# Kernel optimization log

Hardware: AMD Instinct MI355X
Metric: run time of the kernel (lower is better)

## Reference

```python
import jax, jax.numpy as jnp
import numpy as np

B, P, T, R, A = 16384, 3, 2, 3, 3   # batch, n_players, teammates, rivals, action_dim
HID = [1024, 512]
ENC_OUT = 64
RIVAL_START = 9 * 9 + 12 * P       # 117, as in the torch module
NEG_SLOPE = 0.01                    # nn.LeakyReLU default


def _linpack(key, k, din, dout):
    # PyTorch nn.Linear default init: U(-1/sqrt(din), 1/sqrt(din))
    kw, kb = jax.random.split(key)
    bound = 1.0 / np.sqrt(din)
    W = jax.random.uniform(kw, (k, din, dout), jnp.float32, -bound, bound)
    b = jax.random.uniform(kb, (k, dout), jnp.float32, -bound, bound)
    return W, b


def setup_inputs() -> dict:
    key = jax.random.key(0)
    ks = jax.random.split(key, 16)
    obs = jax.random.normal(ks[0], (B, P, 144), jnp.float32)
    act = jax.random.normal(ks[1], (B, P, A), jnp.float32)
    # stacked per-segment encoder weights (grouped small GEMMs)
    Wp1, bp1 = _linpack(ks[2], 9, 2 + A, 32)
    Wp2, bp2 = _linpack(ks[3], 9, 32, ENC_OUT)
    Wt1, bt1 = _linpack(ks[4], T, 12, 32)
    Wt2, bt2 = _linpack(ks[5], T, 32, ENC_OUT)
    Wr1, br1 = _linpack(ks[6], R, 9, 32)
    Wr2, br2 = _linpack(ks[7], R, 32, ENC_OUT)
    # q head: [P*896] -> 1024 -> 512 -> P
    din = P * (9 + T + R) * ENC_OUT
    Wq1, bq1 = _linpack(ks[8], 1, din, HID[0]);  Wq1, bq1 = Wq1[0], bq1[0]
    Wq2, bq2 = _linpack(ks[9], 1, HID[0], HID[1]); Wq2, bq2 = Wq2[0], bq2[0]
    Wq3, bq3 = _linpack(ks[10], 1, HID[1], P);   Wq3, bq3 = Wq3[0], bq3[0]
    return dict(obs=obs, act=act,
                Wp1=Wp1, bp1=bp1, Wp2=Wp2, bp2=bp2,
                Wt1=Wt1, bt1=bt1, Wt2=Wt2, bt2=bt2,
                Wr1=Wr1, br1=br1, Wr2=Wr2, br2=br2,
                Wq1=Wq1, bq1=bq1, Wq2=Wq2, bq2=bq2, Wq3=Wq3, bq3=bq3)


def _enc2(x, W1, b1, W2, b2):
    # x: [B, P, K, din]; W1: [K, din, 32]; W2: [K, 32, 64] -> [B, P, K, 64]
    lrelu = lambda v: jax.nn.leaky_relu(v, NEG_SLOPE)
    h = lrelu(jnp.einsum('bpki,kio->bpko', x, W1) + b1)
    return lrelu(jnp.einsum('bpkh,kho->bpko', h, W2) + b2)


def reference(obs, act, Wp1, bp1, Wp2, bp2, Wt1, bt1, Wt2, bt2,
              Wr1, br1, Wr2, br2, Wq1, bq1, Wq2, bq2, Wq3, bq3):
    b = obs.shape[0]
    # prop segments: obs[:, :, 2i:2i+2] concat act  -> [B, P, 9, 2+A]
    x_prop = jnp.concatenate(
        [obs[:, :, :18].reshape(b, P, 9, 2),
         jnp.broadcast_to(act[:, :, None, :], (b, P, 9, A))], axis=-1)
    x_team = obs[:, :, 18:18 + 12 * T].reshape(b, P, T, 12)
    x_riv = obs[:, :, RIVAL_START:RIVAL_START + 9 * R].reshape(b, P, R, 9)
    ep = _enc2(x_prop, Wp1, bp1, Wp2, bp2)   # [B, P, 9, 64]
    et = _enc2(x_team, Wt1, bt1, Wt2, bt2)   # [B, P, T, 64]
    er = _enc2(x_riv, Wr1, br1, Wr2, br2)    # [B, P, R, 64]
    enc = jnp.concatenate([ep, et, er], axis=2).reshape(b, -1)  # [B, P*14*64]
    # q head: ReLU hidden activations, identity output
    h = jax.nn.relu(enc @ Wq1 + bq1)
    h = jax.nn.relu(h @ Wq2 + bq2)
    return h @ Wq3 + bq3                      # [B, P]
```

## Files before the change

kernel.cpp:

```cpp
#include <hip/hip_runtime.h>
#include <hip/hip_bf16.h>
#include <cstdint>

typedef __bf16 bf16x8 __attribute__((ext_vector_type(8)));
typedef float f32x4 __attribute__((ext_vector_type(4)));

__device__ __forceinline__ void gld16(const __bf16* g, __bf16* lds) {
    __builtin_amdgcn_global_load_lds(
        (__attribute__((address_space(1))) void*)(uintptr_t)g,
        (__attribute__((address_space(3))) void*)(uint32_t)(uintptr_t)lds,
        16, 0, 0);
}

__global__ __launch_bounds__(256) void transpose_bf16_k(const float* __restrict__ in,
                                                        __bf16* __restrict__ out,
                                                        int R, int C) {
    __shared__ float t[64][65];
    const int r0 = blockIdx.x * 64, c0 = blockIdx.y * 64;
    const int tid = threadIdx.x;
#pragma unroll
    for (int i = 0; i < 16; i++) {
        int idx = i * 256 + tid;
        int rr = idx >> 6, cc = idx & 63;
        t[rr][cc] = in[(size_t)(r0 + rr) * C + (c0 + cc)];
    }
    __syncthreads();
#pragma unroll
    for (int i = 0; i < 16; i++) {
        int idx = i * 256 + tid;
        int rr = idx >> 6, cc = idx & 63;
        out[(size_t)(c0 + rr) * R + (r0 + cc)] = (__bf16)t[cc][rr];
    }
}

__global__ __launch_bounds__(256) void pack_weights(const float* __restrict__ Wp1, const float* __restrict__ bp1,
                                                    const float* __restrict__ Wp2, const float* __restrict__ bp2,
                                                    const float* __restrict__ Wt1, const float* __restrict__ bt1,
                                                    const float* __restrict__ Wt2, const float* __restrict__ bt2,
                                                    const float* __restrict__ Wr1, const float* __restrict__ br1,
                                                    const float* __restrict__ Wr2, const float* __restrict__ br2,
                                                    float* __restrict__ w1p, __bf16* __restrict__ w2t) {
    const int s = blockIdx.x, tid = threadIdx.x;
    int ks, din, w1off;
    const float *W1, *B1, *W2, *B2;
    if (s < 9)      { ks = s;      din = 5;  w1off = s * 160;
                      W1 = Wp1; B1 = bp1; W2 = Wp2; B2 = bp2; }
    else if (s < 11){ ks = s - 9;  din = 12; w1off = 1440 + ks * 384;
                      W1 = Wt1; B1 = bt1; W2 = Wt2; B2 = bt2; }
    else            { ks = s - 11; din = 9;  w1off = 2208 + ks * 288;
                      W1 = Wr1; B1 = br1; W2 = Wr2; B2 = br2; }
    W1 += ks * din * 32; B1 += ks * 32; W2 += ks * 2048; B2 += ks * 64;
    for (int i = tid; i < din * 32; i += 256) w1p[w1off + i] = W1[i];
    if (tid < 32) w1p[3072 + s * 32 + tid] = B1[tid];
    if (tid < 64) w1p[3520 + s * 64 + tid] = B2[tid];
    for (int i = tid; i < 2048; i += 256) {
        const int o = i >> 5, k = i & 31;
        w2t[s * 2048 + i] = (__bf16)W2[k * 64 + o];
    }
}

__global__ __launch_bounds__(256) void enc_fused(const float* __restrict__ obs,
                                                 const float* __restrict__ act,
                                                 const float* __restrict__ w1p,
                                                 const __bf16* __restrict__ w2t,
                                                 __bf16* __restrict__ enc) {
    __shared__ float sW[4416];
    __shared__ __bf16 sH[2][64 * 40];
    const int tid = threadIdx.x;
    for (int i = tid; i < 4416; i += 256) sW[i] = w1p[i];
    const int rloc = tid >> 2, q = tid & 3;
    const int row = blockIdx.x * 64 + rloc;
    const float* orow = obs + (size_t)row * 144;
    const float a0 = act[row * 3], a1 = act[row * 3 + 1], a2 = act[row * 3 + 2];
    const int wv = tid >> 6, lane = tid & 63;
    const int fr = lane & 15, kq = lane >> 4;
    __syncthreads();
    int buf = 0;

    auto l2 = [&](int s) {
        __syncthreads();
        bf16x8 bfr[4];
#pragma unroll
        for (int n = 0; n < 4; n++)
            bfr[n] = *(const bf16x8*)&w2t[(s * 64 + n * 16 + fr) * 32 + kq * 8];
        const bf16x8 afr = *(const bf16x8*)&sH[buf][(wv * 16 + fr) * 40 + kq * 8];
        f32x4 acc[4] = {};
#pragma unroll
        for (int n = 0; n < 4; n++)
            acc[n] = __builtin_amdgcn_mfma_f32_16x16x32_bf16(afr, bfr[n], acc[n], 0, 0, 0);
        const float* b2 = sW + 3520 + s * 64;
        const size_t rG = (size_t)blockIdx.x * 64 + wv * 16 + kq * 4;
#pragma unroll
        for (int n = 0; n < 4; n++) {
            const float bv = b2[n * 16 + fr];
#pragma unroll
            for (int rg = 0; rg < 4; rg++) {
                float v = acc[n][rg] + bv;
                v = fmaxf(v, 0.01f * v);
                enc[(rG + rg) * 896 + s * 64 + n * 16 + fr] = (__bf16)v;
            }
        }
        buf ^= 1;
    };

#define L1(DIN, W1OFF, SGI, XLOAD)                                   \
    {                                                                \
        float x[DIN];                                                \
        XLOAD;                                                       \
        const float* w1 = sW + (W1OFF);                              \
        const float* b1 = sW + 3072 + (SGI) * 32;                    \
        bf16x8 t_;                                                   \
        _Pragma("unroll") for (int j = 0; j < 8; j++) {              \
            const int o = q * 8 + j;                                 \
            float a_ = b1[o];                                        \
            _Pragma("unroll") for (int i = 0; i < DIN; i++)          \
                a_ += x[i] * w1[i * 32 + o];                         \
            t_[j] = (__bf16)fmaxf(a_, 0.01f * a_);                   \
        }                                                            \
        *(bf16x8*)&sH[buf][rloc * 40 + q * 8] = t_;                  \
    }

    for (int k = 0; k < 9; k++) {
        L1(5, k * 160, k,
           { x[0] = orow[2 * k]; x[1] = orow[2 * k + 1]; x[2] = a0; x[3] = a1; x[4] = a2; })
        l2(k);
    }
    for (int k = 0; k < 2; k++) {
        L1(12, 1440 + k * 384, 9 + k,
           { _Pragma("unroll") for (int i = 0; i < 12; i++) x[i] = orow[18 + 12 * k + i]; })
        l2(9 + k);
    }
    for (int k = 0; k < 3; k++) {
        L1(9, 2208 + k * 288, 11 + k,
           { _Pragma("unroll") for (int i = 0; i < 9; i++) x[i] = orow[117 + 9 * k + i]; })
        l2(11 + k);
    }
#undef L1
}

template <int NB>
__global__ __launch_bounds__(512, 2) void gemm256_relu(const __bf16* __restrict__ Ag,
                                                       const __bf16* __restrict__ Btg,
                                                       const float* __restrict__ bias,
                                                       __bf16* __restrict__ Cg,
                                                       int N, int K, int lgn) {
    __shared__ __align__(16) __bf16 ldsA[2][2][128 * 64];
    __shared__ __align__(16) __bf16 ldsB[2][2][NB * 64 * 64];
    const int tid = threadIdx.x;
    const int wid = tid >> 6, lane = tid & 63;
    const int wm = wid >> 2, wn = wid & 3;
    const int fr = lane & 15, kq = lane >> 4;

    const int chunk = gridDim.x >> 3;
    const int wg = (blockIdx.x & 7) * chunk + (blockIdx.x >> 3);
    const int bn = wg & ((1 << lgn) - 1), bm = wg >> lgn;

    const int c0 = tid, c1 = tid + 512;
    const int r0 = c0 >> 3, s0 = (c0 & 7) ^ (r0 & 7);
    const int r1 = c1 >> 3, s1 = (c1 & 7) ^ (r1 & 7);
    const size_t aH = (size_t)128 * K;
    const size_t bH = (size_t)(NB * 64) * K;
    const __bf16* aB0 = Ag + (size_t)(bm * 256 + r0) * K + s0 * 8;
    const __bf16* aB1 = Ag + (size_t)(bm * 256 + r1) * K + s1 * 8;
    const __bf16* bB0 = Btg + (size_t)(bn * (NB * 128) + r0) * K + s0 * 8;
    const __bf16* bB1 = Btg + (size_t)(bn * (NB * 128) + r1) * K + s1 * 8;

    f32x4 acc[2][2][4][NB] = {};
    bf16x8 a0[4][2], a1[4][2], b0[NB][2], b1[NB][2];

#define STAGE_A(BUF, H, KO)                                   \
    do {                                                      \
        __bf16* d_ = &ldsA[BUF][H][0];                        \
        gld16(aB0 + (H)*aH + (KO), d_ + c0 * 8);              \
        gld16(aB1 + (H)*aH + (KO), d_ + c1 * 8);              \
    } while (0)
#define STAGE_B(BUF, H, KO)                                   \
    do {                                                      \
        __bf16* d_ = &ldsB[BUF][H][0];                        \
        gld16(bB0 + (H)*bH + (KO), d_ + c0 * 8);              \
        if constexpr (NB == 2) gld16(bB1 + (H)*bH + (KO), d_ + c1 * 8); \
    } while (0)

#define LDFA(BUF, H, ROW, KS) \
    (*(const bf16x8*)&ldsA[BUF][H][(ROW) * 64 + ((((KS)*4 + kq) ^ ((ROW)&7)) * 8)])
#define LDFB(BUF, H, ROW, KS) \
    (*(const bf16x8*)&ldsB[BUF][H][(ROW) * 64 + ((((KS)*4 + kq) ^ ((ROW)&7)) * 8)])

#define LOAD_A(BUF, H, DST)                                   \
    _Pragma("unroll") for (int m = 0; m < 4; m++)             \
        _Pragma("unroll") for (int ks = 0; ks < 2; ks++)      \
            DST[m][ks] = LDFA(BUF, H, wm * 64 + m * 16 + fr, ks);
#define LOAD_B(BUF, H, DST)                                   \
    _Pragma("unroll") for (int n = 0; n < NB; n++)            \
        _Pragma("unroll") for (int ks = 0; ks < 2; ks++)      \
            DST[n][ks] = LDFB(BUF, H, wn * (NB * 16) + n * 16 + fr, ks);

#define MM(Q, R, AR, BR)                                      \
    __builtin_amdgcn_s_setprio(1);                            \
    _Pragma("unroll") for (int ks = 0; ks < 2; ks++)          \
        _Pragma("unroll") for (int m = 0; m < 4; m++)         \
            _Pragma("unroll") for (int n = 0; n < NB; n++)    \
                acc[Q][R][m][n] = __builtin_amdgcn_mfma_f32_16x16x32_bf16( \
                    AR[m][ks], BR[n][ks], acc[Q][R][m][n], 0, 0, 0); \
    __builtin_amdgcn_s_setprio(0);

#define SB0 __builtin_amdgcn_sched_barrier(0)
#define BAR __builtin_amdgcn_s_barrier()
#define LGKM_B1                                               \
    if constexpr (NB == 2) asm volatile("s_waitcnt lgkmcnt(4)" ::: "memory"); \
    else asm volatile("s_waitcnt lgkmcnt(2)" ::: "memory");
#define LGKM(NSTR) asm volatile("s_waitcnt lgkmcnt(" NSTR ")" ::: "memory")
#define VMW(NSTR) asm volatile("s_waitcnt vmcnt(" NSTR ")" ::: "memory")
#define VMW2(N2, N1)                                          \
    if constexpr (NB == 2) VMW(#N2); else VMW(#N1);

    const int NT = K >> 6;

    STAGE_A(0, 0, 0);
    STAGE_B(0, 0, 0);
    STAGE_B(0, 1, 0);
    STAGE_A(0, 1, 0);
    VMW("2");
    BAR;
    LOAD_A(0, 0, a0)
    LOAD_B(0, 0, b0)
    SB0;

    for (int t = 0; t < NT - 1; ++t) {
        const int buf = t & 1, nb = buf ^ 1;
        const int kO = (t + 1) << 6;

        STAGE_A(nb, 0, kO);
        STAGE_B(nb, 0, kO);
        VMW2(4, 3);
        LOAD_B(buf, 1, b1)
        SB0;
        BAR;
        LGKM_B1;
        SB0;
        MM(0, 0, a0, b0)

        STAGE_B(nb, 1, kO);
        STAGE_A(nb, 1, kO);
        LOAD_A(buf, 1, a1)
        SB0;
        BAR;
        LGKM("8");
        SB0;
        MM(0, 1, a0, b1)

        BAR;
        LGKM("0");
        SB0;
        MM(1, 0, a1, b0)

        VMW("2");
        BAR;
        LOAD_A(nb, 0, a0)
        LOAD_B(nb, 0, b0)
        SB0;
        MM(1, 1, a1, b1)
    }

    {
        const int buf = (NT - 1) & 1;
        VMW("0");
        LOAD_B(buf, 1, b1)
        SB0;
        BAR;
        LGKM_B1;
        SB0;
        MM(0, 0, a0, b0)

        LOAD_A(buf, 1, a1)
        SB0;
        BAR;
        LGKM("8");
        SB0;
        MM(0, 1, a0, b1)

        BAR;
        LGKM("0");
        SB0;
        MM(1, 0, a1, b0)

        MM(1, 1, a1, b1)
    }

    const int cc = lane & 15, rr = (lane >> 4) << 2;
#pragma unroll
    for (int q = 0; q < 2; q++)
#pragma unroll
        for (int r2 = 0; r2 < 2; r2++)
#pragma unroll
            for (int m = 0; m < 4; m++)
#pragma unroll
                for (int n = 0; n < NB; n++) {
                    const int colG = bn * (NB * 128) + r2 * (NB * 64) + wn * (NB * 16) + n * 16 + cc;
                    const int rowG = bm * 256 + q * 128 + wm * 64 + m * 16 + rr;
                    const float bv = bias[colG];
#pragma unroll
                    for (int reg = 0; reg < 4; reg++) {
                        float v = acc[q][r2][m][n][reg] + bv;
                        v = fmaxf(v, 0.0f);
                        Cg[(size_t)(rowG + reg) * N + colG] = (__bf16)v;
                    }
                }
#undef STAGE_A
#undef STAGE_B
#undef LDFA
#undef LDFB
#undef LOAD_A
#undef LOAD_B
#undef MM
#undef SB0
#undef BAR
#undef LGKM_B1
#undef LGKM
#undef VMW
#undef VMW2
}

__global__ __launch_bounds__(256) void head_kernel(const __bf16* __restrict__ h2,
                                                   const float* __restrict__ Wq3,
                                                   const float* __restrict__ bq3,
                                                   float* __restrict__ out) {
    const int wave = threadIdx.x >> 6, lane = threadIdx.x & 63;
    const int row = blockIdx.x * 4 + wave;
    const bf16x8 hv = *(const bf16x8*)(h2 + (size_t)row * 512 + lane * 8);
    float s0 = 0.f, s1 = 0.f, s2 = 0.f;
#pragma unroll
    for (int i = 0; i < 8; i++) {
        const float hf = (float)hv[i];
        const int k = lane * 8 + i;
        s0 += hf * Wq3[k * 3 + 0];
        s1 += hf * Wq3[k * 3 + 1];
        s2 += hf * Wq3[k * 3 + 2];
    }
#pragma unroll
    for (int off = 32; off > 0; off >>= 1) {
        s0 += __shfl_xor(s0, off);
        s1 += __shfl_xor(s1, off);
        s2 += __shfl_xor(s2, off);
    }
    if (lane == 0) {
        float* o = out + (size_t)row * 3;
        o[0] = s0 + bq3[0];
        o[1] = s1 + bq3[1];
        o[2] = s2 + bq3[2];
    }
}

extern "C" void kernel_launch(void* const* d_in, const int* in_sizes, int n_in,
                              void* d_out, int out_size, void* d_ws, size_t ws_size,
                              hipStream_t stream) {
    const float* obs = (const float*)d_in[0];
    const float* act = (const float*)d_in[1];
    const float* Wp1 = (const float*)d_in[2];  const float* bp1 = (const float*)d_in[3];
    const float* Wp2 = (const float*)d_in[4];  const float* bp2 = (const float*)d_in[5];
    const float* Wt1 = (const float*)d_in[6];  const float* bt1 = (const float*)d_in[7];
    const float* Wt2 = (const float*)d_in[8];  const float* bt2 = (const float*)d_in[9];
    const float* Wr1 = (const float*)d_in[10]; const float* br1 = (const float*)d_in[11];
    const float* Wr2 = (const float*)d_in[12]; const float* br2 = (const float*)d_in[13];
    const float* Wq1 = (const float*)d_in[14]; const float* bq1 = (const float*)d_in[15];
    const float* Wq2 = (const float*)d_in[16]; const float* bq2 = (const float*)d_in[17];
    const float* Wq3 = (const float*)d_in[18]; const float* bq3 = (const float*)d_in[19];
    float* out = (float*)d_out;

    char* ws = (char*)d_ws;
    __bf16* enc = (__bf16*)(ws);
    __bf16* h1  = (__bf16*)(ws + 88080384);
    __bf16* h2  = (__bf16*)(ws + 88080384 + 33554432);
    __bf16* w1t = (__bf16*)(ws + 138412032);
    __bf16* w2t = (__bf16*)(ws + 143917056);
    float*  w1p = (float*)(ws + 144965632);
    __bf16* w2e = (__bf16*)(ws + 144983296);

    pack_weights<<<14, 256, 0, stream>>>(Wp1, bp1, Wp2, bp2, Wt1, bt1, Wt2, bt2,
                                         Wr1, br1, Wr2, br2, w1p, w2e);
    transpose_bf16_k<<<dim3(2688 / 64, 1024 / 64), 256, 0, stream>>>(Wq1, w1t, 2688, 1024);
    transpose_bf16_k<<<dim3(1024 / 64, 512 / 64), 256, 0, stream>>>(Wq2, w2t, 1024, 512);

    enc_fused<<<768, 256, 0, stream>>>(obs, act, w1p, w2e, enc);

    gemm256_relu<2><<<dim3(256), 512, 0, stream>>>(enc, w1t, bq1, h1, 1024, 2688, 2);
    gemm256_relu<1><<<dim3(256), 512, 0, stream>>>(h1, w2t, bq2, h2, 512, 1024, 2);
    head_kernel<<<16384 / 4, 256, 0, stream>>>(h2, Wq3, bq3, out);
}
```

Before: 146.9 us.

## Merge weight prep kernels and pipeline encoder stages with LDS-staged coalesced stores

```diff
diff --git a/kernel.cpp b/kernel.cpp
--- a/kernel.cpp
+++ b/kernel.cpp
@@ -12,50 +12,53 @@
         16, 0, 0);
 }
 
-__global__ __launch_bounds__(256) void transpose_bf16_k(const float* __restrict__ in,
-                                                        __bf16* __restrict__ out,
-                                                        int R, int C) {
+__global__ __launch_bounds__(256) void prep_all(const float* __restrict__ Wq1, const float* __restrict__ Wq2,
+                                                const float* __restrict__ Wp1, const float* __restrict__ bp1,
+                                                const float* __restrict__ Wp2, const float* __restrict__ bp2,
+                                                const float* __restrict__ Wt1, const float* __restrict__ bt1,
+                                                const float* __restrict__ Wt2, const float* __restrict__ bt2,
+                                                const float* __restrict__ Wr1, const float* __restrict__ br1,
+                                                const float* __restrict__ Wr2, const float* __restrict__ br2,
+                                                __bf16* __restrict__ w1t, __bf16* __restrict__ w2t,
+                                                float* __restrict__ w1p, __bf16* __restrict__ w2e) {
     __shared__ float t[64][65];
-    const int r0 = blockIdx.x * 64, c0 = blockIdx.y * 64;
-    const int tid = threadIdx.x;
-#pragma unroll
-    for (int i = 0; i < 16; i++) {
-        int idx = i * 256 + tid;
-        int rr = idx >> 6, cc = idx & 63;
-        t[rr][cc] = in[(size_t)(r0 + rr) * C + (c0 + cc)];
-    }
-    __syncthreads();
-#pragma unroll
-    for (int i = 0; i < 16; i++) {
-        int idx = i * 256 + tid;
-        int rr = idx >> 6, cc = idx & 63;
-        out[(size_t)(c0 + rr) * R + (r0 + cc)] = (__bf16)t[cc][rr];
-    }
-}
-
-__global__ __launch_bounds__(256) void pack_weights(const float* __restrict__ Wp1, const float* __restrict__ bp1,
-                                                    const float* __restrict__ Wp2, const float* __restrict__ bp2,
-                                                    const float* __restrict__ Wt1, const float* __restrict__ bt1,
-                                                    const float* __restrict__ Wt2, const float* __restrict__ bt2,
-                                                    const float* __restrict__ Wr1, const float* __restrict__ br1,
-                                                    const float* __restrict__ Wr2, const float* __restrict__ br2,
-                                                    float* __restrict__ w1p, __bf16* __restrict__ w2t) {
-    const int s = blockIdx.x, tid = threadIdx.x;
-    int ks, din, w1off;
-    const float *W1, *B1, *W2, *B2;
-    if (s < 9)      { ks = s;      din = 5;  w1off = s * 160;
-                      W1 = Wp1; B1 = bp1; W2 = Wp2; B2 = bp2; }
-    else if (s < 11){ ks = s - 9;  din = 12; w1off = 1440 + ks * 384;
-                      W1 = Wt1; B1 = bt1; W2 = Wt2; B2 = bt2; }
-    else            { ks = s - 11; din = 9;  w1off = 2208 + ks * 288;
-                      W1 = Wr1; B1 = br1; W2 = Wr2; B2 = br2; }
-    W1 += ks * din * 32; B1 += ks * 32; W2 += ks * 2048; B2 += ks * 64;
-    for (int i = tid; i < din * 32; i += 256) w1p[w1off + i] = W1[i];
-    if (tid < 32) w1p[3072 + s * 32 + tid] = B1[tid];
-    if (tid < 64) w1p[3520 + s * 64 + tid] = B2[tid];
-    for (int i = tid; i < 2048; i += 256) {
-        const int o = i >> 5, k = i & 31;
-        w2t[s * 2048 + i] = (__bf16)W2[k * 64 + o];
+    const int idx = blockIdx.x, tid = threadIdx.x;
+    if (idx < 800) {
+        const float* in; __bf16* out; int R, C, bx, by;
+        if (idx < 672) { in = Wq1; out = w1t; R = 2688; C = 1024; bx = idx % 42; by = idx / 42; }
+        else { const int i2 = idx - 672; in = Wq2; out = w2t; R = 1024; C = 512; bx = i2 % 16; by = i2 / 16; }
+        const int r0 = bx * 64, c0 = by * 64;
+#pragma unroll
+        for (int i = 0; i < 16; i++) {
+            int id2 = i * 256 + tid;
+            int rr = id2 >> 6, cc = id2 & 63;
+            t[rr][cc] = in[(size_t)(r0 + rr) * C + (c0 + cc)];
+        }
+        __syncthreads();
+#pragma unroll
+        for (int i = 0; i < 16; i++) {
+            int id2 = i * 256 + tid;
+            int rr = id2 >> 6, cc = id2 & 63;
+            out[(size_t)(c0 + rr) * R + (r0 + cc)] = (__bf16)t[cc][rr];
+        }
+    } else {
+        const int s = idx - 800;
+        int ks, din, w1off;
+        const float *W1, *B1, *W2, *B2;
+        if (s < 9)      { ks = s;      din = 5;  w1off = s * 160;
+                          W1 = Wp1; B1 = bp1; W2 = Wp2; B2 = bp2; }
+        else if (s < 11){ ks = s - 9;  din = 12; w1off = 1440 + ks * 384;
+                          W1 = Wt1; B1 = bt1; W2 = Wt2; B2 = bt2; }
+        else            { ks = s - 11; din = 9;  w1off = 2208 + ks * 288;
+                          W1 = Wr1; B1 = br1; W2 = Wr2; B2 = br2; }
+        W1 += ks * din * 32; B1 += ks * 32; W2 += ks * 2048; B2 += ks * 64;
+        for (int i = tid; i < din * 32; i += 256) w1p[w1off + i] = W1[i];
+        if (tid < 32) w1p[3072 + s * 32 + tid] = B1[tid];
+        if (tid < 64) w1p[3520 + s * 64 + tid] = B2[tid];
+        for (int i = tid; i < 2048; i += 256) {
+            const int o = i >> 5, k = i & 31;
+            w2e[s * 2048 + i] = (__bf16)W2[k * 64 + o];
+        }
     }
 }
 
@@ -66,6 +69,7 @@
                                                  __bf16* __restrict__ enc) {
     __shared__ float sW[4416];
     __shared__ __bf16 sH[2][64 * 40];
+    __shared__ __align__(16) __bf16 sO[2][64 * 72];
     const int tid = threadIdx.x;
     for (int i = tid; i < 4416; i += 256) sW[i] = w1p[i];
     const int rloc = tid >> 2, q = tid & 3;
@@ -74,22 +78,31 @@
     const float a0 = act[row * 3], a1 = act[row * 3 + 1], a2 = act[row * 3 + 2];
     const int wv = tid >> 6, lane = tid & 63;
     const int fr = lane & 15, kq = lane >> 4;
-    __syncthreads();
-    int buf = 0;
-
-    auto l2 = [&](int s) {
-        __syncthreads();
-        bf16x8 bfr[4];
+
+    bf16x8 bfrA[4], bfrB[4];
+    int curH = 0, curO = 0;
+
+    auto prefetchB = [&](int sn) {
 #pragma unroll
         for (int n = 0; n < 4; n++)
-            bfr[n] = *(const bf16x8*)&w2t[(s * 64 + n * 16 + fr) * 32 + kq * 8];
-        const bf16x8 afr = *(const bf16x8*)&sH[buf][(wv * 16 + fr) * 40 + kq * 8];
+            bfrB[n] = *(const bf16x8*)&w2t[(sn * 64 + n * 16 + fr) * 32 + kq * 8];
+    };
+    auto storeOut = [&](int sp, int bO) {
+#pragma unroll
+        for (int h = 0; h < 2; h++) {
+            const int c = tid + h * 256;
+            const int r = c >> 3, ch = c & 7;
+            const bf16x8 v = *(const bf16x8*)&sO[bO][r * 72 + ch * 8];
+            *(bf16x8*)&enc[((size_t)blockIdx.x * 64 + r) * 896 + sp * 64 + ch * 8] = v;
+        }
+    };
+    auto l2c = [&](int s, int bH, int bO) {
+        const bf16x8 afr = *(const bf16x8*)&sH[bH][(wv * 16 + fr) * 40 + kq * 8];
         f32x4 acc[4] = {};
 #pragma unroll
         for (int n = 0; n < 4; n++)
-            acc[n] = __builtin_amdgcn_mfma_f32_16x16x32_bf16(afr, bfr[n], acc[n], 0, 0, 0);
+            acc[n] = __builtin_amdgcn_mfma_f32_16x16x32_bf16(afr, bfrA[n], acc[n], 0, 0, 0);
         const float* b2 = sW + 3520 + s * 64;
-        const size_t rG = (size_t)blockIdx.x * 64 + wv * 16 + kq * 4;
 #pragma unroll
         for (int n = 0; n < 4; n++) {
             const float bv = b2[n * 16 + fr];
@@ -97,13 +110,12 @@
             for (int rg = 0; rg < 4; rg++) {
                 float v = acc[n][rg] + bv;
                 v = fmaxf(v, 0.01f * v);
-                enc[(rG + rg) * 896 + s * 64 + n * 16 + fr] = (__bf16)v;
+                sO[bO][(wv * 16 + kq * 4 + rg) * 72 + n * 16 + fr] = (__bf16)v;
             }
         }
-        buf ^= 1;
     };
 
-#define L1(DIN, W1OFF, SGI, XLOAD)                                   \
+#define L1(DIN, W1OFF, SGI, DH, XLOAD)                               \
     {                                                                \
         float x[DIN];                                                \
         XLOAD;                                                       \
@@ -117,25 +129,50 @@
                 a_ += x[i] * w1[i * 32 + o];                         \
             t_[j] = (__bf16)fmaxf(a_, 0.01f * a_);                   \
         }                                                            \
-        *(bf16x8*)&sH[buf][rloc * 40 + q * 8] = t_;                  \
-    }
-
-    for (int k = 0; k < 9; k++) {
-        L1(5, k * 160, k,
-           { x[0] = orow[2 * k]; x[1] = orow[2 * k + 1]; x[2] = a0; x[3] = a1; x[4] = a2; })
-        l2(k);
-    }
-    for (int k = 0; k < 2; k++) {
-        L1(12, 1440 + k * 384, 9 + k,
-           { _Pragma("unroll") for (int i = 0; i < 12; i++) x[i] = orow[18 + 12 * k + i]; })
-        l2(9 + k);
-    }
-    for (int k = 0; k < 3; k++) {
-        L1(9, 2208 + k * 288, 11 + k,
-           { _Pragma("unroll") for (int i = 0; i < 9; i++) x[i] = orow[117 + 9 * k + i]; })
-        l2(11 + k);
-    }
+        *(bf16x8*)&sH[DH][rloc * 40 + q * 8] = t_;                   \
+    }
+
+#define PROPX(K) { x[0] = orow[2 * (K)]; x[1] = orow[2 * (K) + 1]; x[2] = a0; x[3] = a1; x[4] = a2; }
+#define TEAMX(K) { _Pragma("unroll") for (int i = 0; i < 12; i++) x[i] = orow[18 + 12 * (K) + i]; }
+#define RIVX(K)  { _Pragma("unroll") for (int i = 0; i < 9; i++) x[i] = orow[117 + 9 * (K) + i]; }
+
+#define STEP(S, NEXTL1)                                              \
+    __syncthreads();                                                 \
+    if ((S) < 13) prefetchB((S) + 1);                                \
+    if ((S) > 0) storeOut((S) - 1, curO ^ 1);                        \
+    l2c((S), curH, curO);                                            \
+    _Pragma("unroll") for (int n = 0; n < 4; n++) bfrA[n] = bfrB[n]; \
+    NEXTL1                                                           \
+    curH ^= 1; curO ^= 1;
+
+    prefetchB(0);
+    __syncthreads();
+#pragma unroll
+    for (int n = 0; n < 4; n++) bfrA[n] = bfrB[n];
+    L1(5, 0, 0, 0, PROPX(0))
+
+    STEP(0,  L1(5, 160, 1, curH ^ 1, PROPX(1)))
+    STEP(1,  L1(5, 320, 2, curH ^ 1, PROPX(2)))
+    STEP(2,  L1(5, 480, 3, curH ^ 1, PROPX(3)))
+    STEP(3,  L1(5, 640, 4, curH ^ 1, PROPX(4)))
+    STEP(4,  L1(5, 800, 5, curH ^ 1, PROPX(5)))
+    STEP(5,  L1(5, 960, 6, curH ^ 1, PROPX(6)))
+    STEP(6,  L1(5, 1120, 7, curH ^ 1, PROPX(7)))
+    STEP(7,  L1(5, 1280, 8, curH ^ 1, PROPX(8)))
+    STEP(8,  L1(12, 1440, 9, curH ^ 1, TEAMX(0)))
+    STEP(9,  L1(12, 1824, 10, curH ^ 1, TEAMX(1)))
+    STEP(10, L1(9, 2208, 11, curH ^ 1, RIVX(0)))
+    STEP(11, L1(9, 2496, 12, curH ^ 1, RIVX(1)))
+    STEP(12, L1(9, 2784, 13, curH ^ 1, RIVX(2)))
+    STEP(13, )
+
+    __syncthreads();
+    storeOut(13, curO ^ 1);
+#undef STEP
 #undef L1
+#undef PROPX
+#undef TEAMX
+#undef RIVX
 }
 
 template <int NB>
@@ -376,10 +413,8 @@
     float*  w1p = (float*)(ws + 144965632);
     __bf16* w2e = (__bf16*)(ws + 144983296);
 
-    pack_weights<<<14, 256, 0, stream>>>(Wp1, bp1, Wp2, bp2, Wt1, bt1, Wt2, bt2,
-                                         Wr1, br1, Wr2, br2, w1p, w2e);
-    transpose_bf16_k<<<dim3(2688 / 64, 1024 / 64), 256, 0, stream>>>(Wq1, w1t, 2688, 1024);
-    transpose_bf16_k<<<dim3(1024 / 64, 512 / 64), 256, 0, stream>>>(Wq2, w2t, 1024, 512);
+    prep_all<<<814, 256, 0, stream>>>(Wq1, Wq2, Wp1, bp1, Wp2, bp2, Wt1, bt1, Wt2, bt2,
+                                      Wr1, br1, Wr2, br2, w1t, w2t, w1p, w2e);
 
     enc_fused<<<768, 256, 0, stream>>>(obs, act, w1p, w2e, enc);
 
```

Measured after the change: 137.8 us. 1.07x faster.
